# Kernel tuning notes

Measured on AMD Instinct MI355X. Metric: run time of the kernel, lower is better.

## Reference

```python
import jax, jax.numpy as jnp
import numpy as np

TEMP = 0.1          # temp1 == base_temperature -> scale factor temp/base = 1
N_VIEW = 100        # max_views


def _select_indices(hard, easy):
    """Deterministic analogue of _hard_anchor_sampling's per-(image,class) pick.
    hard, easy: [M, HW] bool. Returns [M, N_VIEW] pixel indices (hard first,
    then easy, in pixel-index order; torch uses randperm but the contrastive
    loss is invariant to which/ordering of in-set samples)."""
    half = N_VIEW // 2
    nh = hard.sum(-1)
    ne = easy.sum(-1)
    both = (nh >= half) & (ne >= half)
    hk = jnp.where(both, half, jnp.where(nh >= half, N_VIEW - ne, nh))  # num_hard_keep
    ek = N_VIEW - hk                                                     # num_easy_keep
    hrank = jnp.cumsum(hard.astype(jnp.int32), -1) - 1
    erank = jnp.cumsum(easy.astype(jnp.int32), -1) - 1
    sel = (hard & (hrank < hk[:, None])) | (easy & (erank < ek[:, None]))
    # stable argsort puts selected pixels first, preserving index order
    order = jnp.argsort(jnp.where(sel, 0, 1), axis=-1)
    return order[:, :N_VIEW]


def _contrastive(feats_, labels_):
    """feats_: [A, V, D], labels_: [A] float. Supervised contrastive loss."""
    A, V, D = feats_.shape
    N = A * V
    # torch.cat(torch.unbind(feats_, 1), 0) -> view-major ordering
    cf = feats_.transpose(1, 0, 2).reshape(N, D)
    lab = jnp.tile(labels_, V)                           # mask.repeat(V, V)
    mask = (lab[:, None] == lab[None, :]).astype(cf.dtype)
    logits = (cf @ cf.T) / TEMP                          # [N, N]
    logits = logits - jax.lax.stop_gradient(logits.max(axis=1, keepdims=True))
    neg_mask = 1.0 - mask                                # before removing diagonal
    pos_mask = mask * (1.0 - jnp.eye(N, dtype=cf.dtype)) # logits_mask zeroes diag
    exp_l = jnp.exp(logits)
    neg_sum = (exp_l * neg_mask).sum(axis=1, keepdims=True)
    log_prob = logits - jnp.log(exp_l + neg_sum)
    mean_log_prob_pos = (pos_mask * log_prob).sum(axis=1) / pos_mask.sum(axis=1)
    return -(TEMP / TEMP) * mean_log_prob_pos.mean()


def _forward(feats, predict, labels):
    B, D, H, W = feats.shape
    C = predict.shape[1]
    HW = H * W
    # F.normalize(feats, p=2, dim=1)
    norm = jnp.sqrt((feats * feats).sum(axis=1, keepdims=True))
    feats = feats / jnp.maximum(norm, 1e-12)
    # bilinear upsample of logits to (H, W), softmax, conf/argmax
    logits_up = jax.image.resize(predict, (B, C, H, W), method='linear')
    probs = jax.nn.softmax(logits_up, axis=1)
    pred = jnp.argmax(probs, axis=1)                     # [B, H, W] (conf unused by loss)
    # nearest resize of labels to (H, W) is identity here (same size)
    pred_f = pred.reshape(B, HW)
    lab_f = labels.reshape(B, HW)
    feats_f = feats.transpose(0, 2, 3, 1).reshape(B, HW, D)
    cls = jnp.arange(C)
    hard = (pred_f[:, None, :] == cls[None, :, None]) & (lab_f[:, None, :] != cls[None, :, None])
    easy = (pred_f[:, None, :] == cls[None, :, None]) & (lab_f[:, None, :] == cls[None, :, None])
    idx = _select_indices(hard.reshape(B * C, HW), easy.reshape(B * C, HW))  # [B*C, N_VIEW]
    b_idx = jnp.repeat(jnp.arange(B), C)
    X_ = feats_f[b_idx[:, None], idx]                    # [B*C, N_VIEW, D]
    y_ = jnp.tile(cls, B).astype(feats.dtype)            # [B*C]
    return _contrastive(X_, y_)


def setup_inputs() -> dict:
    key = jax.random.key(0)
    k1, k2, k3 = jax.random.split(key, 3)
    feats = jax.random.normal(k1, (4, 256, 128, 128), dtype=jnp.float32)
    predict = jax.random.normal(k2, (4, 21, 64, 64), dtype=jnp.float32)
    labels = jax.random.randint(k3, (4, 128, 128), 0, 21, dtype=jnp.int32)
    return {"feats": feats, "predict": predict, "labels": labels}


def reference(feats, predict, labels):
    return _forward(feats, predict, labels)
```

## Files before the change

### kernel.cpp

```cpp
#include <hip/hip_runtime.h>
#include <math.h>

#define HW 16384
#define WID 128
#define BB 4
#define CC 21
#define DD 256
#define NA 84
#define NV 100
#define NN 8400
#define NPOS 400
#define NPAD 8448
#define NTILE 66
#define NSQ (NTILE * NTILE)
#define NPOSBLK (16 * CC)

typedef __bf16 bf16;
typedef bf16 v8bf __attribute__((ext_vector_type(8)));
typedef float v4f __attribute__((ext_vector_type(4)));

#define AS1(p) ((const __attribute__((address_space(1))) void*)(p))
#define AS3(p) ((__attribute__((address_space(3))) void*)(p))

__global__ void pred_kernel(const float* __restrict__ predict, int* __restrict__ pred) {
  int t = blockIdx.x * blockDim.x + threadIdx.x;
  int b = t / HW;
  int p = t % HW;
  int y = p / WID, x = p % WID;
  float yin = y * 0.5f - 0.25f;
  float xin = x * 0.5f - 0.25f;
  int y0 = (int)floorf(yin), x0 = (int)floorf(xin);
  float fy = yin - (float)y0, fx = xin - (float)x0;
  int y0c = max(y0, 0), y1c = min(y0 + 1, 63);
  int x0c = max(x0, 0), x1c = min(x0 + 1, 63);
  float w00 = (1.f - fy) * (1.f - fx), w01 = (1.f - fy) * fx;
  float w10 = fy * (1.f - fx),        w11 = fy * fx;
  const float* pb = predict + (size_t)b * CC * 4096;
  float best = -1e30f; int bc = 0;
  for (int c = 0; c < CC; ++c) {
    const float* pc = pb + c * 4096;
    float v = w00 * pc[y0c * 64 + x0c] + w01 * pc[y0c * 64 + x1c]
            + w10 * pc[y1c * 64 + x0c] + w11 * pc[y1c * 64 + x1c];
    if (v > best) { best = v; bc = c; }
  }
  pred[t] = bc;
}

__global__ __launch_bounds__(256) void select_kernel(const int* __restrict__ pred,
                                                     const int* __restrict__ labels,
                                                     int* __restrict__ idx) {
  int pair = blockIdx.x;
  int b = pair / CC, c = pair % CC;
  int tid = threadIdx.x;
  const int4* pb = (const int4*)(pred + b * HW) + tid * 16;
  const int4* lb = (const int4*)(labels + b * HW) + tid * 16;

  unsigned long long hm = 0ull, em = 0ull;
  #pragma unroll
  for (int g = 0; g < 16; ++g) {
    int4 p4 = pb[g];
    int4 l4 = lb[g];
    unsigned long long h =
        ((unsigned long long)((p4.x == c) & (l4.x != c)))      |
        ((unsigned long long)((p4.y == c) & (l4.y != c)) << 1) |
        ((unsigned long long)((p4.z == c) & (l4.z != c)) << 2) |
        ((unsigned long long)((p4.w == c) & (l4.w != c)) << 3);
    unsigned long long e =
        ((unsigned long long)((p4.x == c) & (l4.x == c)))      |
        ((unsigned long long)((p4.y == c) & (l4.y == c)) << 1) |
        ((unsigned long long)((p4.z == c) & (l4.z == c)) << 2) |
        ((unsigned long long)((p4.w == c) & (l4.w == c)) << 3);
    hm |= h << (g * 4);
    em |= e << (g * 4);
  }
  int nh_t = __popcll(hm), ne_t = __popcll(em);

  __shared__ int sh[256], se[256], ss[256];
  sh[tid] = nh_t; se[tid] = ne_t;
  __syncthreads();
  for (int off = 1; off < 256; off <<= 1) {
    int vh = (tid >= off) ? sh[tid - off] : 0;
    int ve = (tid >= off) ? se[tid - off] : 0;
    __syncthreads();
    sh[tid] += vh; se[tid] += ve;
    __syncthreads();
  }
  int h_excl = sh[tid] - nh_t, e_excl = se[tid] - ne_t;
  int nh = sh[255], ne = se[255];

  const int half = NV / 2;
  int hk;
  if (nh >= half && ne >= half) hk = half;
  else if (nh >= half)          hk = NV - ne;
  else                          hk = nh;
  int ek = NV - hk;

  int takeh = min(max(hk - h_excl, 0), nh_t);
  int takee = min(max(ek - e_excl, 0), ne_t);
  int sel_t = takeh + takee;
  ss[tid] = sel_t;
  __syncthreads();
  for (int off = 1; off < 256; off <<= 1) {
    int vs = (tid >= off) ? ss[tid - off] : 0;
    __syncthreads();
    ss[tid] += vs;
    __syncthreads();
  }
  int s_excl = ss[tid] - sel_t;
  int total_sel = ss[255];
  int F = NV - total_sel;
  int u_excl = tid * 64 - s_excl;

  int* out = idx + pair * NV;
  int sc = 0, uc = 0, hc = 0, ec = 0;
  for (int l = 0; l < 64; ++l) {
    int p = tid * 64 + l;
    int hard = (int)((hm >> l) & 1ull);
    int easy = (int)((em >> l) & 1ull);
    bool sel = (hard && hc < takeh) || (easy && ec < takee);
    hc += hard; ec += easy;
    if (sel) {
      if (s_excl + sc < NV) out[s_excl + sc] = p;
      sc++;
    } else {
      if (u_excl + uc < F) out[total_sel + u_excl + uc] = p;
      uc++;
    }
  }
}

__global__ __launch_bounds__(256) void gather_kernel(const float* __restrict__ feats,
                                                     const int* __restrict__ idx,
                                                     bf16* __restrict__ cf) {
  int g = blockIdx.x;
  int a = g % NA;
  int v0 = (g / NA) * 4;
  int b = a / CC;
  int d = threadIdx.x;

  int p[4];
  #pragma unroll
  for (int k = 0; k < 4; ++k) p[k] = idx[a * NV + v0 + k];
  const float* base = feats + (size_t)(b * DD + d) * HW;
  float val[4], ssk[4];
  #pragma unroll
  for (int k = 0; k < 4; ++k) { val[k] = base[p[k]]; ssk[k] = val[k] * val[k]; }

  #pragma unroll
  for (int k = 0; k < 4; ++k) {
    float s = ssk[k];
    s += __shfl_xor(s, 1);  s += __shfl_xor(s, 2);  s += __shfl_xor(s, 4);
    s += __shfl_xor(s, 8);  s += __shfl_xor(s, 16); s += __shfl_xor(s, 32);
    ssk[k] = s;
  }
  __shared__ float red[4][4];
  if ((d & 63) == 0) {
    #pragma unroll
    for (int k = 0; k < 4; ++k) red[d >> 6][k] = ssk[k];
  }
  __syncthreads();
  #pragma unroll
  for (int k = 0; k < 4; ++k) {
    float tot = red[0][k] + red[1][k] + red[2][k] + red[3][k];
    float inv = 1.0f / fmaxf(sqrtf(tot), 1e-12f);
    int n = (v0 + k) * NA + a;
    cf[(size_t)n * DD + d] = (bf16)(val[k] * inv);
  }
}

__global__ __launch_bounds__(256) void gemm_kernel(const bf16* __restrict__ cf,
                                                   float* __restrict__ row_part,
                                                   float* __restrict__ s_pos) {
  __shared__ __align__(16) bf16 smem[2 * 128 * 64];
  bf16* sA = smem;
  bf16* sB = smem + 128 * 64;
  int blk = blockIdx.x;
  bool pos = blk >= NSQ;
  int i0, j0, c = 0;
  if (!pos) {
    i0 = (blk / NTILE) * 128;
    j0 = (blk % NTILE) * 128;
  } else {
    int pb = blk - NSQ;
    c = pb / 16;
    int bx = pb % 16;
    i0 = (bx >> 2) * 128;
    j0 = (bx & 3) * 128;
  }
  int tid = threadIdx.x;
  int wave = tid >> 6, lane = tid & 63;
  int wi = wave >> 1, wj = wave & 1;
  int m = lane & 15, q = lane >> 4;

  v4f acc[4][4] = {};

  int lrow = lane >> 3;
  int cxor = (lane & 7) ^ lrow;

  for (int k0 = 0; k0 < DD; k0 += 64) {
    #pragma unroll
    for (int it = 0; it < 4; ++it) {
      int row = wave * 32 + it * 8;
      int ri = i0 + row + lrow, rj = j0 + row + lrow;
      int gi, gj;
      if (!pos) { gi = ri; gj = rj; }
      else {
        gi = (ri < NPOS) ? ((ri >> 2) * NA + (ri & 3) * CC + c) : NN;
        gj = (rj < NPOS) ? ((rj >> 2) * NA + (rj & 3) * CC + c) : NN;
      }
      const bf16* gA = cf + (size_t)gi * DD + k0 + cxor * 8;
      const bf16* gB = cf + (size_t)gj * DD + k0 + cxor * 8;
      __builtin_amdgcn_global_load_lds(AS1(gA), AS3(sA + row * 64), 16, 0, 0);
      __builtin_amdgcn_global_load_lds(AS1(gB), AS3(sB + row * 64), 16, 0, 0);
    }
    __syncthreads();
    #pragma unroll
    for (int kk = 0; kk < 2; ++kk) {
      v8bf af[4], bfr[4];
      #pragma unroll
      for (int tt = 0; tt < 4; ++tt) {
        int r = wi * 64 + tt * 16 + m;
        af[tt] = *(const v8bf*)(sA + r * 64 + (((kk * 4 + q) ^ (m & 7)) * 8));
      }
      #pragma unroll
      for (int tt = 0; tt < 4; ++tt) {
        int r = wj * 64 + tt * 16 + m;
        bfr[tt] = *(const v8bf*)(sB + r * 64 + (((kk * 4 + q) ^ (m & 7)) * 8));
      }
      #pragma unroll
      for (int ti = 0; ti < 4; ++ti)
        #pragma unroll
        for (int tj = 0; tj < 4; ++tj)
          acc[ti][tj] = __builtin_amdgcn_mfma_f32_16x16x32_bf16(af[ti], bfr[tj], acc[ti][tj], 0, 0, 0);
    }
    __syncthreads();
  }

  if (!pos) {
    int jw0 = j0 + wj * 64;
    float rowp[16];
    #pragma unroll
    for (int tt = 0; tt < 16; ++tt) rowp[tt] = 0.f;

    #pragma unroll
    for (int ti = 0; ti < 4; ++ti) {
      #pragma unroll
      for (int r = 0; r < 4; ++r) {
        #pragma unroll
        for (int tj = 0; tj < 4; ++tj) {
          int j = jw0 + tj * 16 + m;
          if (j >= NN) continue;
          rowp[ti * 4 + r] += __expf(acc[ti][tj][r] * 10.0f - 10.0f);
        }
      }
    }

    float* red = (float*)smem;
    #pragma unroll
    for (int ti = 0; ti < 4; ++ti)
      #pragma unroll
      for (int r = 0; r < 4; ++r) {
        int rg = wi * 64 + ti * 16 + q * 4 + r;
        red[rg * 33 + wj * 16 + m] = rowp[ti * 4 + r];
      }
    __syncthreads();
    if (tid < 128) {
      float s = 0.f;
      #pragma unroll
      for (int t = 0; t < 32; ++t) s += red[tid * 33 + t];
      row_part[(size_t)(blk % NTILE) * NPAD + i0 + tid] = s;
    }
  } else {
    #pragma unroll
    for (int ti = 0; ti < 4; ++ti) {
      #pragma unroll
      for (int r = 0; r < 4; ++r) {
        int ri = i0 + wi * 64 + ti * 16 + q * 4 + r;
        if (ri >= NPOS) continue;
        int gi = (ri >> 2) * NA + (ri & 3) * CC + c;
        #pragma unroll
        for (int tj = 0; tj < 4; ++tj) {
          int rj = j0 + wj * 64 + tj * 16 + m;
          if (rj < NPOS)
            s_pos[(size_t)gi * NPOS + rj] = acc[ti][tj][r] * 10.0f - 10.0f;
        }
      }
    }
  }
}

__global__ __launch_bounds__(256) void loss_kernel(const float* __restrict__ s_pos,
                                                   const float* __restrict__ row_part,
                                                   double* __restrict__ partials) {
  int tid = threadIdx.x;
  int wave = tid >> 6, lane = tid & 63;
  int i = blockIdx.x * 4 + wave;
  const float* row = s_pos + (size_t)i * NPOS;

  float nsum = 0.f;
  for (int jb = lane; jb < NTILE; jb += 64)
    nsum += row_part[(size_t)jb * NPAD + i];

  float sp[7], ev[7];
  float psum = 0.f;
  #pragma unroll
  for (int t = 0; t < 7; ++t) {
    int k = lane + t * 64;
    if (k < NPOS) {
      sp[t] = row[k];
      ev[t] = __expf(sp[t]);
      psum += ev[t];
    } else { sp[t] = 0.f; ev[t] = 0.f; }
  }
  float comb = nsum - psum;
  for (int o = 32; o; o >>= 1) comb += __shfl_xor(comb, o);
  float ns = comb;

  int self = (i / NA) * 4 + ((i % NA) / CC);
  float tsum = 0.f;
  #pragma unroll
  for (int t = 0; t < 7; ++t) {
    int k = lane + t * 64;
    if (k < NPOS && k != self)
      tsum += sp[t] - __logf(ev[t] + ns);
  }
  for (int o = 32; o; o >>= 1) tsum += __shfl_xor(tsum, o);

  __shared__ float r2[4];
  if (lane == 0) r2[wave] = tsum;
  __syncthreads();
  if (tid == 0) partials[blockIdx.x] = (double)(r2[0] + r2[1] + r2[2] + r2[3]);
}

__global__ void final_kernel(const double* __restrict__ partials, float* __restrict__ out) {
  int lane = threadIdx.x;
  double s = 0.0;
  for (int t = lane; t < 2100; t += 64) s += partials[t];
  for (int o = 32; o; o >>= 1) s += __shfl_down(s, o);
  if (lane == 0) out[0] = (float)(-s / 399.0 / 8400.0);
}

extern "C" void kernel_launch(void* const* d_in, const int* in_sizes, int n_in,
                              void* d_out, int out_size, void* d_ws, size_t ws_size,
                              hipStream_t stream) {
  const float* feats   = (const float*)d_in[0];
  const float* predict = (const float*)d_in[1];
  const int*   labels  = (const int*)d_in[2];
  float* out = (float*)d_out;
  char* ws = (char*)d_ws;

  int*    pred     = (int*)(ws + 0);
  int*    idx      = (int*)(ws + 262144);
  float*  row_part = (float*)(ws + 295744);
  double* partials = (double*)(ws + 2526016);
  bf16*   cf       = (bf16*)(ws + 2542816);
  float*  s_pos    = (float*)(ws + 6868192);

  (void)hipMemsetAsync((char*)(cf + (size_t)NN * DD), 0, (size_t)(NPAD - NN) * DD * 2, stream);

  pred_kernel<<<256, 256, 0, stream>>>(predict, pred);
  select_kernel<<<NA, 256, 0, stream>>>(pred, labels, idx);
  gather_kernel<<<2100, 256, 0, stream>>>(feats, idx, cf);
  gemm_kernel<<<NSQ + NPOSBLK, 256, 0, stream>>>(cf, row_part, s_pos);
  loss_kernel<<<2100, 256, 0, stream>>>(s_pos, row_part, partials);
  final_kernel<<<1, 64, 0, stream>>>(partials, out);
}
```

Baseline: 204.8 us.

## Widen GEMM tiles to 128x256 and restructure gather to stage features in LDS

The similarity GEMM now computes 128x256 output tiles per block, so each block has twice the accumulators and B-tile LDS footprint, and the grid shrinks from 66x66 to 66x33 tiles plus fewer positive-pair blocks. This is meant to cut A-tile reloads and improve MFMA-to-load ratio, but it raises register and LDS use and may lower occupancy. The gather kernel is rewritten to handle 50 views per block, staging the feature columns in padded shared memory, normalising them, and writing 16-byte vectorised bf16 rows instead of scattered 2-byte stores. Workspace offsets shrink to match the smaller row_part buffer.

```diff
diff --git a/kernel.cpp b/kernel.cpp
--- a/kernel.cpp
+++ b/kernel.cpp
@@ -11,9 +11,10 @@
 #define NN 8400
 #define NPOS 400
 #define NPAD 8448
-#define NTILE 66
-#define NSQ (NTILE * NTILE)
-#define NPOSBLK (16 * CC)
+#define NIT 66
+#define NJT 33
+#define NNEG (NIT * NJT)
+#define NPOSB (CC * 8)
 
 typedef __bf16 bf16;
 typedef bf16 v8bf __attribute__((ext_vector_type(8)));
@@ -132,67 +133,80 @@
 __global__ __launch_bounds__(256) void gather_kernel(const float* __restrict__ feats,
                                                      const int* __restrict__ idx,
                                                      bf16* __restrict__ cf) {
-  int g = blockIdx.x;
-  int a = g % NA;
-  int v0 = (g / NA) * 4;
-  int b = a / CC;
-  int d = threadIdx.x;
-
-  int p[4];
-  #pragma unroll
-  for (int k = 0; k < 4; ++k) p[k] = idx[a * NV + v0 + k];
-  const float* base = feats + (size_t)(b * DD + d) * HW;
-  float val[4], ssk[4];
-  #pragma unroll
-  for (int k = 0; k < 4; ++k) { val[k] = base[p[k]]; ssk[k] = val[k] * val[k]; }
-
-  #pragma unroll
-  for (int k = 0; k < 4; ++k) {
-    float s = ssk[k];
-    s += __shfl_xor(s, 1);  s += __shfl_xor(s, 2);  s += __shfl_xor(s, 4);
-    s += __shfl_xor(s, 8);  s += __shfl_xor(s, 16); s += __shfl_xor(s, 32);
-    ssk[k] = s;
-  }
-  __shared__ float red[4][4];
-  if ((d & 63) == 0) {
-    #pragma unroll
-    for (int k = 0; k < 4; ++k) red[d >> 6][k] = ssk[k];
-  }
-  __syncthreads();
-  #pragma unroll
-  for (int k = 0; k < 4; ++k) {
-    float tot = red[0][k] + red[1][k] + red[2][k] + red[3][k];
-    float inv = 1.0f / fmaxf(sqrtf(tot), 1e-12f);
-    int n = (v0 + k) * NA + a;
-    cf[(size_t)n * DD + d] = (bf16)(val[k] * inv);
+  __shared__ float fv[50 * 257];
+  __shared__ float ssp[4][64];
+  __shared__ float inv_s[50];
+  int blkid = blockIdx.x;
+  int pair = blkid >> 1;
+  int vhalf = blkid & 1;
+  int b = pair / CC;
+  int t = threadIdx.x;
+  int px = t & 63;
+  int dgrp = t >> 6;
+
+  int p = 0;
+  if (px < 50) p = idx[pair * NV + vhalf * 50 + px];
+  const float* base = feats + ((size_t)b * DD + dgrp * 64) * HW;
+
+  float ss = 0.f;
+  if (px < 50) {
+    #pragma unroll 4
+    for (int dd = 0; dd < 64; ++dd) {
+      float val = base[(size_t)dd * HW + p];
+      fv[px * 257 + dgrp * 64 + dd] = val;
+      ss += val * val;
+    }
+  }
+  ssp[dgrp][px] = ss;
+  __syncthreads();
+  if (t < 50) {
+    float tot = ssp[0][t] + ssp[1][t] + ssp[2][t] + ssp[3][t];
+    inv_s[t] = 1.0f / fmaxf(sqrtf(tot), 1e-12f);
+  }
+  __syncthreads();
+
+  int rsub = t >> 5;
+  int c8 = (t & 31) * 8;
+  for (int pass = 0; pass < 7; ++pass) {
+    int r = pass * 8 + rsub;
+    if (r < 50) {
+      float inv = inv_s[r];
+      int n = (vhalf * 50 + r) * NA + pair;
+      v8bf o;
+      #pragma unroll
+      for (int k = 0; k < 8; ++k)
+        o[k] = (bf16)(fv[r * 257 + c8 + k] * inv);
+      *(v8bf*)(cf + (size_t)n * DD + c8) = o;
+    }
   }
 }
 
 __global__ __launch_bounds__(256) void gemm_kernel(const bf16* __restrict__ cf,
                                                    float* __restrict__ row_part,
                                                    float* __restrict__ s_pos) {
-  __shared__ __align__(16) bf16 smem[2 * 128 * 64];
+  __shared__ __align__(16) bf16 smem[(128 + 256) * 64];
   bf16* sA = smem;
   bf16* sB = smem + 128 * 64;
   int blk = blockIdx.x;
-  bool pos = blk >= NSQ;
-  int i0, j0, c = 0;
+  bool pos = blk >= NNEG;
+  int i0, j0, c = 0, jb = 0;
   if (!pos) {
-    i0 = (blk / NTILE) * 128;
-    j0 = (blk % NTILE) * 128;
+    jb = blk % NJT;
+    i0 = (blk / NJT) * 128;
+    j0 = jb * 256;
   } else {
-    int pb = blk - NSQ;
-    c = pb / 16;
-    int bx = pb % 16;
-    i0 = (bx >> 2) * 128;
-    j0 = (bx & 3) * 128;
+    int pb = blk - NNEG;
+    c = pb >> 3;
+    int loc = pb & 7;
+    i0 = (loc >> 1) * 128;
+    j0 = (loc & 1) * 256;
   }
   int tid = threadIdx.x;
   int wave = tid >> 6, lane = tid & 63;
   int wi = wave >> 1, wj = wave & 1;
   int m = lane & 15, q = lane >> 4;
 
-  v4f acc[4][4] = {};
+  v4f acc[4][8] = {};
 
   int lrow = lane >> 3;
   int cxor = (lane & 7) ^ lrow;
@@ -201,43 +215,44 @@
     #pragma unroll
     for (int it = 0; it < 4; ++it) {
       int row = wave * 32 + it * 8;
-      int ri = i0 + row + lrow, rj = j0 + row + lrow;
-      int gi, gj;
-      if (!pos) { gi = ri; gj = rj; }
-      else {
-        gi = (ri < NPOS) ? ((ri >> 2) * NA + (ri & 3) * CC + c) : NN;
-        gj = (rj < NPOS) ? ((rj >> 2) * NA + (rj & 3) * CC + c) : NN;
-      }
-      const bf16* gA = cf + (size_t)gi * DD + k0 + cxor * 8;
-      const bf16* gB = cf + (size_t)gj * DD + k0 + cxor * 8;
-      __builtin_amdgcn_global_load_lds(AS1(gA), AS3(sA + row * 64), 16, 0, 0);
-      __builtin_amdgcn_global_load_lds(AS1(gB), AS3(sB + row * 64), 16, 0, 0);
+      int ri = i0 + row + lrow;
+      int gi = !pos ? ri : ((ri < NPOS) ? ((ri >> 2) * NA + (ri & 3) * CC + c) : NN);
+      __builtin_amdgcn_global_load_lds(AS1(cf + (size_t)gi * DD + k0 + cxor * 8),
+                                       AS3(sA + row * 64), 16, 0, 0);
+    }
+    #pragma unroll
+    for (int it = 0; it < 8; ++it) {
+      int row = wave * 64 + it * 8;
+      int rj = j0 + row + lrow;
+      int gj = !pos ? rj : ((rj < NPOS) ? ((rj >> 2) * NA + (rj & 3) * CC + c) : NN);
+      __builtin_amdgcn_global_load_lds(AS1(cf + (size_t)gj * DD + k0 + cxor * 8),
+                                       AS3(sB + row * 64), 16, 0, 0);
     }
     __syncthreads();
     #pragma unroll
     for (int kk = 0; kk < 2; ++kk) {
-      v8bf af[4], bfr[4];
+      v8bf af[4], bfr[8];
       #pragma unroll
       for (int tt = 0; tt < 4; ++tt) {
         int r = wi * 64 + tt * 16 + m;
         af[tt] = *(const v8bf*)(sA + r * 64 + (((kk * 4 + q) ^ (m & 7)) * 8));
       }
       #pragma unroll
-      for (int tt = 0; tt < 4; ++tt) {
-        int r = wj * 64 + tt * 16 + m;
+      for (int tt = 0; tt < 8; ++tt) {
+        int r = wj * 128 + tt * 16 + m;
         bfr[tt] = *(const v8bf*)(sB + r * 64 + (((kk * 4 + q) ^ (m & 7)) * 8));
       }
       #pragma unroll
       for (int ti = 0; ti < 4; ++ti)
         #pragma unroll
-        for (int tj = 0; tj < 4; ++tj)
+        for (int tj = 0; tj < 8; ++tj)
           acc[ti][tj] = __builtin_amdgcn_mfma_f32_16x16x32_bf16(af[ti], bfr[tj], acc[ti][tj], 0, 0, 0);
     }
     __syncthreads();
   }
 
   if (!pos) {
-    int jw0 = j0 + wj * 64;
+    int jw0 = j0 + wj * 128;
     float rowp[16];
     #pragma unroll
     for (int tt = 0; tt < 16; ++tt) rowp[tt] = 0.f;
@@ -247,7 +262,7 @@
       #pragma unroll
       for (int r = 0; r < 4; ++r) {
         #pragma unroll
-        for (int tj = 0; tj < 4; ++tj) {
+        for (int tj = 0; tj < 8; ++tj) {
           int j = jw0 + tj * 16 + m;
           if (j >= NN) continue;
           rowp[ti * 4 + r] += __expf(acc[ti][tj][r] * 10.0f - 10.0f);
@@ -268,7 +283,7 @@
       float s = 0.f;
       #pragma unroll
       for (int t = 0; t < 32; ++t) s += red[tid * 33 + t];
-      row_part[(size_t)(blk % NTILE) * NPAD + i0 + tid] = s;
+      row_part[(size_t)jb * NPAD + i0 + tid] = s;
     }
   } else {
     #pragma unroll
@@ -279,8 +294,8 @@
         if (ri >= NPOS) continue;
         int gi = (ri >> 2) * NA + (ri & 3) * CC + c;
         #pragma unroll
-        for (int tj = 0; tj < 4; ++tj) {
-          int rj = j0 + wj * 64 + tj * 16 + m;
+        for (int tj = 0; tj < 8; ++tj) {
+          int rj = j0 + wj * 128 + tj * 16 + m;
           if (rj < NPOS)
             s_pos[(size_t)gi * NPOS + rj] = acc[ti][tj][r] * 10.0f - 10.0f;
         }
@@ -298,7 +313,7 @@
   const float* row = s_pos + (size_t)i * NPOS;
 
   float nsum = 0.f;
-  for (int jb = lane; jb < NTILE; jb += 64)
+  for (int jb = lane; jb < NJT; jb += 64)
     nsum += row_part[(size_t)jb * NPAD + i];
 
   float sp[7], ev[7];
@@ -352,16 +367,16 @@
   int*    pred     = (int*)(ws + 0);
   int*    idx      = (int*)(ws + 262144);
   float*  row_part = (float*)(ws + 295744);
-  double* partials = (double*)(ws + 2526016);
-  bf16*   cf       = (bf16*)(ws + 2542816);
-  float*  s_pos    = (float*)(ws + 6868192);
+  double* partials = (double*)(ws + 1410880);
+  bf16*   cf       = (bf16*)(ws + 1427680);
+  float*  s_pos    = (float*)(ws + 5753056);
 
   (void)hipMemsetAsync((char*)(cf + (size_t)NN * DD), 0, (size_t)(NPAD - NN) * DD * 2, stream);
 
   pred_kernel<<<256, 256, 0, stream>>>(predict, pred);
   select_kernel<<<NA, 256, 0, stream>>>(pred, labels, idx);
-  gather_kernel<<<2100, 256, 0, stream>>>(feats, idx, cf);
-  gemm_kernel<<<NSQ + NPOSBLK, 256, 0, stream>>>(cf, row_part, s_pos);
+  gather_kernel<<<168, 256, 0, stream>>>(feats, idx, cf);
+  gemm_kernel<<<NNEG + NPOSB, 256, 0, stream>>>(cf, row_part, s_pos);
   loss_kernel<<<2100, 256, 0, stream>>>(s_pos, row_part, partials);
   final_kernel<<<1, 64, 0, stream>>>(partials, out);
 }
```

Result: slower. 246.7 us (+20.4%).

## Exploit Gram matrix symmetry with triangular tile grid and fold padding memset into gather

Applied to the files above, without the earlier changes.

The similarity GEMM now launches only lower-triangular 128x128 tiles and decodes the tile coordinates from the block index with a sqrt. Each off-diagonal tile writes both its row partial sums and, through an extra LDS reduction, its column partial sums into the transposed slot of row_part. This roughly halves the MFMA and exp work of the NxN pass. The separate memset of the padding rows is replaced by an extra block in the gather kernel, which removes one API call, at the cost of more epilogue reduction work per tile.

```diff
diff --git a/kernel.cpp b/kernel.cpp
--- a/kernel.cpp
+++ b/kernel.cpp
@@ -12,7 +12,7 @@
 #define NPOS 400
 #define NPAD 8448
 #define NTILE 66
-#define NSQ (NTILE * NTILE)
+#define NTRI 2211
 #define NPOSBLK (16 * CC)
 
 typedef __bf16 bf16;
@@ -133,10 +133,16 @@
                                                      const int* __restrict__ idx,
                                                      bf16* __restrict__ cf) {
   int g = blockIdx.x;
+  int d = threadIdx.x;
+  if (g == 2100) {
+    v8bf z = {};
+    for (int e = d; e < (NPAD - NN) * DD / 8; e += 256)
+      *(v8bf*)(cf + (size_t)NN * DD + e * 8) = z;
+    return;
+  }
   int a = g % NA;
   int v0 = (g / NA) * 4;
   int b = a / CC;
-  int d = threadIdx.x;
 
   int p[4];
   #pragma unroll
@@ -175,13 +181,19 @@
   bf16* sA = smem;
   bf16* sB = smem + 128 * 64;
   int blk = blockIdx.x;
-  bool pos = blk >= NSQ;
-  int i0, j0, c = 0;
+  bool pos = blk >= NTRI;
+  int i0, j0, c = 0, I = 0, J = 0;
+  bool diag = false;
   if (!pos) {
-    i0 = (blk / NTILE) * 128;
-    j0 = (blk % NTILE) * 128;
+    I = (int)((sqrtf(8.0f * blk + 1.0f) - 1.0f) * 0.5f);
+    while ((I + 1) * (I + 2) / 2 <= blk) ++I;
+    while (I * (I + 1) / 2 > blk) --I;
+    J = blk - I * (I + 1) / 2;
+    i0 = I * 128;
+    j0 = J * 128;
+    diag = (I == J);
   } else {
-    int pb = blk - NSQ;
+    int pb = blk - NTRI;
     c = pb / 16;
     int bx = pb % 16;
     i0 = (bx >> 2) * 128;
@@ -208,10 +220,10 @@
         gi = (ri < NPOS) ? ((ri >> 2) * NA + (ri & 3) * CC + c) : NN;
         gj = (rj < NPOS) ? ((rj >> 2) * NA + (rj & 3) * CC + c) : NN;
       }
-      const bf16* gA = cf + (size_t)gi * DD + k0 + cxor * 8;
-      const bf16* gB = cf + (size_t)gj * DD + k0 + cxor * 8;
-      __builtin_amdgcn_global_load_lds(AS1(gA), AS3(sA + row * 64), 16, 0, 0);
-      __builtin_amdgcn_global_load_lds(AS1(gB), AS3(sB + row * 64), 16, 0, 0);
+      __builtin_amdgcn_global_load_lds(AS1(cf + (size_t)gi * DD + k0 + cxor * 8),
+                                       AS3(sA + row * 64), 16, 0, 0);
+      __builtin_amdgcn_global_load_lds(AS1(cf + (size_t)gj * DD + k0 + cxor * 8),
+                                       AS3(sB + row * 64), 16, 0, 0);
     }
     __syncthreads();
     #pragma unroll
@@ -237,8 +249,10 @@
   }
 
   if (!pos) {
+    int iw0 = i0 + wi * 64;
     int jw0 = j0 + wj * 64;
     float rowp[16];
+    float colp[4] = {0.f, 0.f, 0.f, 0.f};
     #pragma unroll
     for (int tt = 0; tt < 16; ++tt) rowp[tt] = 0.f;
 
@@ -246,29 +260,46 @@
     for (int ti = 0; ti < 4; ++ti) {
       #pragma unroll
       for (int r = 0; r < 4; ++r) {
+        int i = iw0 + ti * 16 + q * 4 + r;
+        bool iok = (i < NN);
         #pragma unroll
         for (int tj = 0; tj < 4; ++tj) {
           int j = jw0 + tj * 16 + m;
-          if (j >= NN) continue;
-          rowp[ti * 4 + r] += __expf(acc[ti][tj][r] * 10.0f - 10.0f);
+          float e = __expf(acc[ti][tj][r] * 10.0f - 10.0f);
+          if (j < NN) rowp[ti * 4 + r] += e;
+          if (!diag && iok) colp[tj] += e;
         }
       }
     }
 
-    float* red = (float*)smem;
+    float* redR = (float*)smem;
+    float* redC = (float*)smem + 128 * 33;
     #pragma unroll
     for (int ti = 0; ti < 4; ++ti)
       #pragma unroll
       for (int r = 0; r < 4; ++r) {
         int rg = wi * 64 + ti * 16 + q * 4 + r;
-        red[rg * 33 + wj * 16 + m] = rowp[ti * 4 + r];
-      }
+        redR[rg * 33 + wj * 16 + m] = rowp[ti * 4 + r];
+      }
+    if (!diag) {
+      #pragma unroll
+      for (int tj = 0; tj < 4; ++tj) {
+        int cg = wj * 64 + tj * 16 + m;
+        redC[cg * 9 + wi * 4 + q] = colp[tj];
+      }
+    }
     __syncthreads();
     if (tid < 128) {
       float s = 0.f;
       #pragma unroll
-      for (int t = 0; t < 32; ++t) s += red[tid * 33 + t];
-      row_part[(size_t)(blk % NTILE) * NPAD + i0 + tid] = s;
+      for (int t = 0; t < 32; ++t) s += redR[tid * 33 + t];
+      row_part[(size_t)J * NPAD + i0 + tid] = s;
+      if (!diag) {
+        float s2 = 0.f;
+        #pragma unroll
+        for (int t = 0; t < 8; ++t) s2 += redC[tid * 9 + t];
+        row_part[(size_t)I * NPAD + j0 + tid] = s2;
+      }
     }
   } else {
     #pragma unroll
@@ -356,12 +387,10 @@
   bf16*   cf       = (bf16*)(ws + 2542816);
   float*  s_pos    = (float*)(ws + 6868192);
 
-  (void)hipMemsetAsync((char*)(cf + (size_t)NN * DD), 0, (size_t)(NPAD - NN) * DD * 2, stream);
-
   pred_kernel<<<256, 256, 0, stream>>>(predict, pred);
   select_kernel<<<NA, 256, 0, stream>>>(pred, labels, idx);
-  gather_kernel<<<2100, 256, 0, stream>>>(feats, idx, cf);
-  gemm_kernel<<<NSQ + NPOSBLK, 256, 0, stream>>>(cf, row_part, s_pos);
+  gather_kernel<<<2101, 256, 0, stream>>>(feats, idx, cf);
+  gemm_kernel<<<NTRI + NPOSBLK, 256, 0, stream>>>(cf, row_part, s_pos);
   loss_kernel<<<2100, 256, 0, stream>>>(s_pos, row_part, partials);
   final_kernel<<<1, 64, 0, stream>>>(partials, out);
 }
```

New measurement: 185.4 us. 1.1x faster.
